# Optimization experiments

Measured on AMD Instinct MI355X. Metric: run time of the kernel, lower is better.

The kernel has to match this reference:

```python
import jax, jax.numpy as jnp
import numpy as np

B, S, D = 2, 2048, 1024
H, DK, DV = 16, 64, 64


def setup_inputs() -> dict:
    key = jax.random.key(0)
    ks = jax.random.split(key, 10)
    scale = 0.02
    return {
        "x": jax.random.normal(ks[0], (B, S, D), dtype=jnp.float32),
        "Wq": jax.random.normal(ks[1], (D, H * DK), dtype=jnp.float32) * scale,
        "bq": jax.random.normal(ks[2], (H * DK,), dtype=jnp.float32) * scale,
        "Wk": jax.random.normal(ks[3], (D, H * DK), dtype=jnp.float32) * scale,
        "bk": jax.random.normal(ks[4], (H * DK,), dtype=jnp.float32) * scale,
        "Wv": jax.random.normal(ks[5], (D, H * DV), dtype=jnp.float32) * scale,
        "bv": jax.random.normal(ks[6], (H * DV,), dtype=jnp.float32) * scale,
        "Wo": jax.random.normal(ks[7], (H * DV, D), dtype=jnp.float32) * scale,
        "bo": jax.random.normal(ks[8], (D,), dtype=jnp.float32) * scale,
    }


def reference(x, Wq, bq, Wk, bk, Wv, bv, Wo, bo):
    b, s, d = x.shape
    # projections -> (b, H, s, dk/dv)
    q = (x @ Wq + bq).reshape(b, s, H, DK).transpose(0, 2, 1, 3)
    k = (x @ Wk + bk).reshape(b, s, H, DK).transpose(0, 2, 1, 3)
    v = (x @ Wv + bv).reshape(b, s, H, DV).transpose(0, 2, 1, 3)
    # scaled QK^T: (b, H, s, s)
    scores = jnp.einsum("bhqd,bhkd->bhqk", q, k) / np.sqrt(DK).astype(np.float32)
    # sign-based reweighting: scores * sign(scores) (zeros -> sign 1) == |scores|
    reweighted = jnp.abs(scores)
    # causal mask: lower triangle keeps value, strict upper -> -inf (value * -inf)
    causal = jnp.tril(jnp.ones((s, s), dtype=bool))
    logits = jnp.where(causal, reweighted, -jnp.inf)
    w = jax.nn.softmax(logits, axis=-1)
    o = jnp.einsum("bhqk,bhkd->bhqd", w, v)  # (b, H, s, DV)
    o = o.transpose(0, 2, 1, 3).reshape(b, s, H * DV)
    return o @ Wo + bo
```

## Files before the change

kernel.cpp:

```cpp
#include <hip/hip_runtime.h>


#define DI __device__ __forceinline__

typedef __bf16 bf16x8 __attribute__((ext_vector_type(8)));
typedef float f32x4 __attribute__((ext_vector_type(4)));
typedef unsigned short u16x8 __attribute__((ext_vector_type(8)));
typedef unsigned short u16x4 __attribute__((ext_vector_type(4)));

union U8 { u16x8 u; bf16x8 b; };
union PB { unsigned int w[4]; u16x8 u; bf16x8 b; };

typedef const __attribute__((address_space(1))) unsigned int* gas_p;
typedef __attribute__((address_space(3))) unsigned int* las_p;

DI void gload16(const unsigned short* g, unsigned short* l) {
  __builtin_amdgcn_global_load_lds((gas_p)(const void*)g, (las_p)(void*)l, 16, 0, 0);
}

#define WAIT_VM4  asm volatile("s_waitcnt vmcnt(4)" ::: "memory")
#define WAIT_VM0  asm volatile("s_waitcnt vmcnt(0)" ::: "memory")
#define BARRIER   __builtin_amdgcn_s_barrier()

DI unsigned short f2bf(float f) {
  unsigned int u = __float_as_uint(f);
  u += 0x7FFFu + ((u >> 16) & 1u);
  return (unsigned short)(u >> 16);
}
DI float bf2f(unsigned short v) { return __uint_as_float((unsigned int)v << 16); }

__global__ __launch_bounds__(256) void k_conv_x(const float* __restrict__ x,
                                                unsigned short* __restrict__ xb) {
  size_t i = ((size_t)blockIdx.x * 256 + threadIdx.x) * 4;
  float4 v = *(const float4*)(x + i);
  u16x4 o;
  o[0] = f2bf(v.x); o[1] = f2bf(v.y); o[2] = f2bf(v.z); o[3] = f2bf(v.w);
  *(u16x4*)(xb + i) = o;
}

__global__ __launch_bounds__(256) void k_transpose(
    const float* __restrict__ W0, const float* __restrict__ W1,
    const float* __restrict__ W2, const float* __restrict__ W3,
    unsigned short* __restrict__ T0, unsigned short* __restrict__ T1,
    unsigned short* __restrict__ T2, unsigned short* __restrict__ T3) {
  const int z = blockIdx.z;
  const float* W = (z == 0) ? W0 : (z == 1) ? W1 : (z == 2) ? W2 : W3;
  unsigned short* T = (z == 0) ? T0 : (z == 1) ? T1 : (z == 2) ? T2 : T3;
  __shared__ unsigned short buf[32][33];
  const int k0 = blockIdx.x * 32, n0 = blockIdx.y * 32;
  const int tx = threadIdx.x, ty = threadIdx.y;
#pragma unroll
  for (int j = 0; j < 4; ++j) {
    int r = ty + j * 8;
    buf[r][tx] = f2bf(W[(size_t)(k0 + r) * 1024 + n0 + tx]);
  }
  __syncthreads();
#pragma unroll
  for (int j = 0; j < 4; ++j) {
    int c = ty + j * 8;
    T[(size_t)(n0 + c) * 1024 + k0 + tx] = buf[tx][c];
  }
}

DI void stage_gemm(const unsigned short* __restrict__ src, unsigned short* dst,
                   int row0, int k0, int tid, int wid) {
#pragma unroll
  for (int i = 0; i < 2; ++i) {
    int T = i * 256 + tid;
    int row = T >> 2, ch = T & 3;
    int sch = ch ^ (row & 3);
    gload16(&src[(size_t)(row0 + row) * 1024 + k0 + sch * 8],
            &dst[(i * 256 + wid * 64) * 8]);
  }
}

DI void gemm_main(const unsigned short* __restrict__ A,
                  const unsigned short* __restrict__ Bm,
                  unsigned short* As, unsigned short* Bs,
                  int m0, int n0, f32x4 acc[4][4]) {
  const int tid = threadIdx.x;
  const int lane = tid & 63, wid = tid >> 6;
  const int wr = wid >> 1, wc = wid & 1;
  const int g = lane >> 4, lq = lane & 15;

  stage_gemm(A, As, m0, 0, tid, wid);
  stage_gemm(Bm, Bs, n0, 0, tid, wid);
  __syncthreads();
  int buf = 0;
  for (int k0 = 0; k0 < 1024; k0 += 32) {
    if (k0 + 32 < 1024) {
      stage_gemm(A, As + (buf ^ 1) * 4096, m0, k0 + 32, tid, wid);
      stage_gemm(Bm, Bs + (buf ^ 1) * 4096, n0, k0 + 32, tid, wid);
    }
    const unsigned short* Ab = As + buf * 4096;
    const unsigned short* Bb = Bs + buf * 4096;
    U8 af[4], bfr[4];
#pragma unroll
    for (int f = 0; f < 4; ++f) {
      af[f].u  = *(const u16x8*)&Ab[(wr * 64 + f * 16 + lq) * 32 + ((g ^ (lq & 3)) * 8)];
      bfr[f].u = *(const u16x8*)&Bb[(wc * 64 + f * 16 + lq) * 32 + ((g ^ (lq & 3)) * 8)];
    }
#pragma unroll
    for (int i = 0; i < 4; ++i)
#pragma unroll
      for (int j = 0; j < 4; ++j)
        acc[i][j] = __builtin_amdgcn_mfma_f32_16x16x32_bf16(af[i].b, bfr[j].b,
                                                            acc[i][j], 0, 0, 0);
    __syncthreads();
    buf ^= 1;
  }
}

__global__ __launch_bounds__(256) void k_gemm_qkv(
    const unsigned short* __restrict__ xb,
    const unsigned short* __restrict__ Wqt, const unsigned short* __restrict__ Wkt,
    const unsigned short* __restrict__ Wvt,
    const float* __restrict__ bq, const float* __restrict__ bk,
    const float* __restrict__ bv,
    unsigned short* __restrict__ Qo, unsigned short* __restrict__ Ko,
    unsigned short* __restrict__ Vto) {
  __shared__ unsigned short Sh[128 * 136];
  unsigned short* As = Sh;
  unsigned short* Bs = Sh + 8192;
  const int z = blockIdx.z;
  const unsigned short* Bm = (z == 0) ? Wqt : (z == 1) ? Wkt : Wvt;
  const float* bias = (z == 0) ? bq : (z == 1) ? bk : bv;

  f32x4 acc[4][4];
#pragma unroll
  for (int i = 0; i < 4; ++i)
#pragma unroll
    for (int j = 0; j < 4; ++j) acc[i][j] = f32x4{0.f, 0.f, 0.f, 0.f};

  const int m0 = blockIdx.x * 128, n0 = blockIdx.y * 128;
  gemm_main(xb, Bm, As, Bs, m0, n0, acc);

  const int tid = threadIdx.x;
  const int lane = tid & 63, wid = tid >> 6;
  const int wr = wid >> 1, wc = wid & 1;
  const int g = lane >> 4, lq = lane & 15;
  const int bb = m0 >> 11;

#pragma unroll
  for (int j = 0; j < 4; ++j) {
    int col = wc * 64 + j * 16 + lq;
    float bv_ = bias[n0 + col];
#pragma unroll
    for (int i = 0; i < 4; ++i)
#pragma unroll
      for (int r = 0; r < 4; ++r) {
        int row = wr * 64 + i * 16 + g * 4 + r;
        Sh[row * 136 + col] = f2bf(acc[i][j][r] + bv_);
      }
  }
  __syncthreads();

  if (z < 2) {
    unsigned short* dstQK = (z == 0) ? Qo : Ko;
    const int ch = tid & 15, sb = tid >> 4;
#pragma unroll
    for (int it = 0; it < 8; ++it) {
      int s = sb + it * 16;
      u16x8 v = *(const u16x8*)&Sh[s * 136 + ch * 8];
      int gcol = n0 + ch * 8;
      int hh = gcol >> 6, dd = gcol & 63;
      int sr = (m0 + s) & 2047;
      *(u16x8*)&dstQK[(((size_t)(bb * 16 + hh)) * 2048 + sr) * 64 + dd] = v;
    }
  } else {
    const int d = tid & 127, hf = tid >> 7;
    int gcol = n0 + d;
    int hh = gcol >> 6, dd = gcol & 63;
    size_t vrow = ((size_t)(bb * 16 + hh)) * 64 + dd;
#pragma unroll
    for (int it = 0; it < 8; ++it) {
      int s0 = (hf + it * 2) * 8;
      u16x8 vv;
#pragma unroll
      for (int e = 0; e < 8; ++e) vv[e] = Sh[(s0 + e) * 136 + d];
      *(u16x8*)&Vto[vrow * 2048 + (m0 & 2047) + s0] = vv;
    }
  }
}

__global__ __launch_bounds__(256) void k_gemm_out(
    const unsigned short* __restrict__ Ob, const unsigned short* __restrict__ Wot,
    const float* __restrict__ bo, float* __restrict__ out) {
  __shared__ unsigned short As[2 * 4096];
  __shared__ unsigned short Bs[2 * 4096];
  f32x4 acc[4][4];
#pragma unroll
  for (int i = 0; i < 4; ++i)
#pragma unroll
    for (int j = 0; j < 4; ++j) acc[i][j] = f32x4{0.f, 0.f, 0.f, 0.f};

  const int m0 = blockIdx.x * 128, n0 = blockIdx.y * 128;
  gemm_main(Ob, Wot, As, Bs, m0, n0, acc);

  const int lane = threadIdx.x & 63, wid = threadIdx.x >> 6;
  const int wr = wid >> 1, wc = wid & 1;
  const int g = lane >> 4, lq = lane & 15;
#pragma unroll
  for (int j = 0; j < 4; ++j) {
    int col = n0 + wc * 64 + j * 16 + lq;
    float bv_ = bo[col];
#pragma unroll
    for (int i = 0; i < 4; ++i)
#pragma unroll
      for (int r = 0; r < 4; ++r) {
        int row = m0 + wr * 64 + i * 16 + g * 4 + r;
        out[(size_t)row * 1024 + col] = acc[i][j][r] + bv_;
      }
  }
}

template<bool MASKED>
DI void ptile(f32x4 sacc[4], f32x4& lacc, unsigned int pk[4][2],
              int qrow, int kk0, int g) {
  const float SC = 0.18033688011112042f;
#pragma unroll
  for (int c = 0; c < 4; ++c) {
#pragma unroll
    for (int r = 0; r < 4; ++r) {
      float sv = fabsf(sacc[c][r]) * SC;
      if (MASKED) {
        int k = kk0 + g * 8 + r + 4 * (c & 1) + 32 * (c >> 1);
        sv = (k <= qrow) ? sv : -1e30f;
      }
      float p = exp2f(sv);
      sacc[c][r] = p;
      lacc[r] += p;
    }
    asm("v_cvt_pk_bf16_f32 %0, %1, %2"
        : "=v"(pk[c][0]) : "v"(sacc[c][0]), "v"(sacc[c][1]));
    asm("v_cvt_pk_bf16_f32 %0, %1, %2"
        : "=v"(pk[c][1]) : "v"(sacc[c][2]), "v"(sacc[c][3]));
  }
}

DI void flash_dual(bool complete, int qblk, int t0, int t1, int slot,
                   const unsigned short* __restrict__ Q,
                   const unsigned short* __restrict__ Km,
                   const unsigned short* __restrict__ Vt,
                   unsigned short* __restrict__ O,
                   unsigned short* __restrict__ Pp, float* __restrict__ Lp,
                   unsigned short* Ks0, unsigned short* Vs0,
                   size_t qkbase, size_t vbase, int b, int h,
                   int tid, int wid, int g, int lq) {
  const int lrowA = wid * 32 + lq, lrowB = lrowA + 16;
  const int qrowA = qblk * 128 + lrowA, qrowB = qblk * 128 + lrowB;
  const int diag0 = 2 * qblk;

  auto stage = [&](int bf, int t) {
    const int kk0 = t * 64;
#pragma unroll
    for (int i = 0; i < 2; ++i) {
      int T = i * 256 + tid;
      int row = T >> 3, ch = T & 7;
      int sch = ch ^ (row & 7);
      gload16(&Km[qkbase + (size_t)(kk0 + row) * 64 + sch * 8],
              Ks0 + bf * 4096 + (i * 2048 + wid * 512));
      gload16(&Vt[vbase + (size_t)row * 2048 + kk0 + sch * 8],
              Vs0 + bf * 4096 + (i * 2048 + wid * 512));
    }
  };

  U8 aqA0, aqA1, aqB0, aqB1;
  {
    const unsigned short* qp = &Q[qkbase + (size_t)qrowA * 64 + g * 8];
    aqA0.u = *(const u16x8*)qp;
    aqA1.u = *(const u16x8*)(qp + 32);
    const unsigned short* qp2 = &Q[qkbase + (size_t)qrowB * 64 + g * 8];
    aqB0.u = *(const u16x8*)qp2;
    aqB1.u = *(const u16x8*)(qp2 + 32);
  }
  f32x4 laccA = f32x4{0.f, 0.f, 0.f, 0.f}, laccB = f32x4{0.f, 0.f, 0.f, 0.f};
  f32x4 oaccA[4], oaccB[4];
#pragma unroll
  for (int c = 0; c < 4; ++c) {
    oaccA[c] = f32x4{0.f, 0.f, 0.f, 0.f};
    oaccB[c] = f32x4{0.f, 0.f, 0.f, 0.f};
  }

  const int rbase = (lq >> 2) * 8 + (lq & 3);

  stage(0, t0);
  if (t0 + 1 < t1) stage(1, t0 + 1);
  int bi = 0;
  for (int t = t0; t < t1; ++t) {
    if (t + 1 < t1) WAIT_VM4; else WAIT_VM0;
    BARRIER;
    if (t + 2 < t1) {
      int nb = bi + 2; if (nb >= 3) nb -= 3;
      stage(nb, t + 2);
    }
    const unsigned short* Kb = Ks0 + bi * 4096;
    const unsigned short* Vb = Vs0 + bi * 4096;
    const int kk0 = t * 64;
    f32x4 saccA[4], saccB[4];
    __builtin_amdgcn_s_setprio(1);
#pragma unroll
    for (int c = 0; c < 4; ++c) {
      int row = rbase + 4 * (c & 1) + 32 * (c >> 1);
      int r7 = row & 7;
      U8 kf0, kf1;
      kf0.u = *(const u16x8*)&Kb[row * 64 + ((g ^ r7) * 8)];
      kf1.u = *(const u16x8*)&Kb[row * 64 + (((4 + g) ^ r7) * 8)];
      saccA[c] = __builtin_amdgcn_mfma_f32_16x16x32_bf16(kf0.b, aqA0.b,
                                                         f32x4{0.f, 0.f, 0.f, 0.f}, 0, 0, 0);
      saccA[c] = __builtin_amdgcn_mfma_f32_16x16x32_bf16(kf1.b, aqA1.b, saccA[c], 0, 0, 0);
      saccB[c] = __builtin_amdgcn_mfma_f32_16x16x32_bf16(kf0.b, aqB0.b,
                                                         f32x4{0.f, 0.f, 0.f, 0.f}, 0, 0, 0);
      saccB[c] = __builtin_amdgcn_mfma_f32_16x16x32_bf16(kf1.b, aqB1.b, saccB[c], 0, 0, 0);
    }
    __builtin_amdgcn_s_setprio(0);
    unsigned int pkA[4][2], pkB[4][2];
    if (t >= diag0) {
      ptile<true>(saccA, laccA, pkA, qrowA, kk0, g);
      ptile<true>(saccB, laccB, pkB, qrowB, kk0, g);
    } else {
      ptile<false>(saccA, laccA, pkA, qrowA, kk0, g);
      ptile<false>(saccB, laccB, pkB, qrowB, kk0, g);
    }
    __builtin_amdgcn_s_setprio(1);
#pragma unroll
    for (int hh = 0; hh < 2; ++hh) {
      PB pbA, pbB;
      pbA.w[0] = pkA[hh * 2 + 0][0]; pbA.w[1] = pkA[hh * 2 + 0][1];
      pbA.w[2] = pkA[hh * 2 + 1][0]; pbA.w[3] = pkA[hh * 2 + 1][1];
      pbB.w[0] = pkB[hh * 2 + 0][0]; pbB.w[1] = pkB[hh * 2 + 0][1];
      pbB.w[2] = pkB[hh * 2 + 1][0]; pbB.w[3] = pkB[hh * 2 + 1][1];
#pragma unroll
      for (int c = 0; c < 4; ++c) {
        U8 vf;
        vf.u = *(const u16x8*)&Vb[(c * 16 + lq) * 64 + (((hh * 4 + g) ^ (lq & 7)) * 8)];
        oaccA[c] = __builtin_amdgcn_mfma_f32_16x16x32_bf16(vf.b, pbA.b, oaccA[c], 0, 0, 0);
        oaccB[c] = __builtin_amdgcn_mfma_f32_16x16x32_bf16(vf.b, pbB.b, oaccB[c], 0, 0, 0);
      }
    }
    __builtin_amdgcn_s_setprio(0);
    ++bi; if (bi >= 3) bi = 0;
  }

  float lsA = (laccA[0] + laccA[1]) + (laccA[2] + laccA[3]);
  lsA += __shfl_xor(lsA, 16, 64);
  lsA += __shfl_xor(lsA, 32, 64);
  float lsB = (laccB[0] + laccB[1]) + (laccB[2] + laccB[3]);
  lsB += __shfl_xor(lsB, 16, 64);
  lsB += __shfl_xor(lsB, 32, 64);
  if (complete) {
    float invA = 1.0f / lsA, invB = 1.0f / lsB;
#pragma unroll
    for (int c = 0; c < 4; ++c) {
      u16x4 ovA, ovB;
#pragma unroll
      for (int r2 = 0; r2 < 4; ++r2) {
        ovA[r2] = f2bf(oaccA[c][r2] * invA);
        ovB[r2] = f2bf(oaccB[c][r2] * invB);
      }
      *(u16x4*)&O[((size_t)(b * 2048 + qrowA)) * 1024 + h * 64 + c * 16 + g * 4] = ovA;
      *(u16x4*)&O[((size_t)(b * 2048 + qrowB)) * 1024 + h * 64 + c * 16 + g * 4] = ovB;
    }
  } else {
    if (g == 0) {
      Lp[slot * 128 + lrowA] = lsA;
      Lp[slot * 128 + lrowB] = lsB;
    }
    size_t pbase = (size_t)slot * 8192;
#pragma unroll
    for (int c = 0; c < 4; ++c) {
      u16x4 ovA, ovB;
#pragma unroll
      for (int r2 = 0; r2 < 4; ++r2) {
        ovA[r2] = f2bf(oaccA[c][r2]);
        ovB[r2] = f2bf(oaccB[c][r2]);
      }
      *(u16x4*)&Pp[pbase + lrowA * 64 + c * 16 + g * 4] = ovA;
      *(u16x4*)&Pp[pbase + lrowB * 64 + c * 16 + g * 4] = ovB;
    }
  }
  WAIT_VM0;
  BARRIER;
}

__global__ __launch_bounds__(256) void k_flash(
    const unsigned short* __restrict__ Q, const unsigned short* __restrict__ Km,
    const unsigned short* __restrict__ Vt, unsigned short* __restrict__ O,
    unsigned short* __restrict__ Pp, float* __restrict__ Lp) {
  __shared__ unsigned short Ks[3 * 4096];
  __shared__ unsigned short Vs[3 * 4096];
  const int tid = threadIdx.x;
  const int lane = tid & 63, wid = tid >> 6;
  const int g = lane >> 4, lq = lane & 15;
  const int bid = blockIdx.x;
  const int xcd = bid & 7, idx = bid >> 3;
  const int bh = xcd * 4 + (idx >> 4);
  const int rr = idx & 15;
  const int p = rr >> 1, sp = rr & 1;
  const int mp = 15 - p;
  const int b = bh >> 4, h = bh & 15;
  const size_t qkbase = (size_t)bh * 2048 * 64;
  const size_t vbase = (size_t)bh * 64 * 2048;

  if (sp == 0) {
    flash_dual(true, p, 0, 2 * p + 2, 0, Q, Km, Vt, O, Pp, Lp,
               Ks, Vs, qkbase, vbase, b, h, tid, wid, g, lq);
    flash_dual(false, mp, 0, 15 - 2 * p, (bh * 8 + p) * 2 + 0, Q, Km, Vt, O, Pp, Lp,
               Ks, Vs, qkbase, vbase, b, h, tid, wid, g, lq);
  } else {
    flash_dual(false, mp, 15 - 2 * p, 32 - 2 * p, (bh * 8 + p) * 2 + 1, Q, Km, Vt, O, Pp, Lp,
               Ks, Vs, qkbase, vbase, b, h, tid, wid, g, lq);
  }
}

__global__ __launch_bounds__(256) void k_combine(
    const unsigned short* __restrict__ Pp, const float* __restrict__ Lp,
    unsigned short* __restrict__ O) {
  int gid = blockIdx.x * 256 + threadIdx.x;
  int dv4 = gid & 15;
  int q   = (gid >> 4) & 127;
  int pi  = (gid >> 11) & 7;
  int bh  = gid >> 14;
  int slot0 = (bh * 8 + pi) * 2;
  size_t base = (size_t)slot0 * 8192 + q * 64 + dv4 * 4;
  u16x4 a = *(const u16x4*)&Pp[base];
  u16x4 c = *(const u16x4*)&Pp[base + 8192];
  float l = Lp[slot0 * 128 + q] + Lp[(slot0 + 1) * 128 + q];
  float inv = 1.0f / l;
  u16x4 o;
#pragma unroll
  for (int r = 0; r < 4; ++r) o[r] = f2bf((bf2f(a[r]) + bf2f(c[r])) * inv);
  int b = bh >> 4, h = bh & 15;
  int srow = (15 - pi) * 128 + q;
  *(u16x4*)&O[((size_t)(b * 2048 + srow)) * 1024 + h * 64 + dv4 * 4] = o;
}

extern "C" void kernel_launch(void* const* d_in, const int* in_sizes, int n_in,
                              void* d_out, int out_size, void* d_ws, size_t ws_size,
                              hipStream_t stream) {
  const float* x  = (const float*)d_in[0];
  const float* Wq = (const float*)d_in[1];
  const float* bq = (const float*)d_in[2];
  const float* Wk = (const float*)d_in[3];
  const float* bk = (const float*)d_in[4];
  const float* Wv = (const float*)d_in[5];
  const float* bv = (const float*)d_in[6];
  const float* Wo = (const float*)d_in[7];
  const float* bo = (const float*)d_in[8];
  float* out = (float*)d_out;

  char* ws = (char*)d_ws;
  const size_t MB = 1024 * 1024;
  unsigned short* xb   = (unsigned short*)(ws + 0 * MB);
  unsigned short* Wqt  = (unsigned short*)(ws + 8 * MB);
  unsigned short* Wkt  = (unsigned short*)(ws + 10 * MB);
  unsigned short* Wvt  = (unsigned short*)(ws + 12 * MB);
  unsigned short* Wot  = (unsigned short*)(ws + 14 * MB);
  unsigned short* Qws  = (unsigned short*)(ws + 16 * MB);
  unsigned short* Kws  = (unsigned short*)(ws + 24 * MB);
  unsigned short* Vtws = (unsigned short*)(ws + 32 * MB);
  unsigned short* Ows  = (unsigned short*)(ws + 40 * MB);
  unsigned short* Pp   = (unsigned short*)(ws + 0 * MB);
  float*          Lp   = (float*)(ws + 8 * MB);

  k_conv_x<<<4096, 256, 0, stream>>>(x, xb);
  k_transpose<<<dim3(32, 32, 4), dim3(32, 8), 0, stream>>>(Wq, Wk, Wv, Wo,
                                                           Wqt, Wkt, Wvt, Wot);
  k_gemm_qkv<<<dim3(32, 8, 3), 256, 0, stream>>>(xb, Wqt, Wkt, Wvt, bq, bk, bv,
                                                 Qws, Kws, Vtws);
  k_flash<<<512, 256, 0, stream>>>(Qws, Kws, Vtws, Ows, Pp, Lp);
  k_combine<<<2048, 256, 0, stream>>>(Pp, Lp, Ows);
  k_gemm_out<<<dim3(32, 8), 256, 0, stream>>>(Ows, Wot, bo, out);
}
```

Measured before the change: 111.7 us.

## Fuse Q, K, V projections into one block sharing the staged x tile

The QKV GEMM kernel now computes all three projections in a single block, staging each x tile once and reusing it against the Wq, Wk and Wv tiles, which cuts x loads by a factor of three. The grid shrinks from 768 to 256 blocks and each thread holds 48 accumulator vectors, so register pressure rises and occupancy drops to one block per CU. On a GPU with 256 CUs this leaves a single wave of work, with less latency hiding. The epilogue stores the three outputs one after another through shared memory.

```diff
diff --git a/kernel.cpp b/kernel.cpp
--- a/kernel.cpp
+++ b/kernel.cpp
@@ -74,6 +74,115 @@
   }
 }
 
+__global__ __launch_bounds__(256, 1) void k_gemm_qkv(
+    const unsigned short* __restrict__ xb,
+    const unsigned short* __restrict__ Wqt, const unsigned short* __restrict__ Wkt,
+    const unsigned short* __restrict__ Wvt,
+    const float* __restrict__ bq, const float* __restrict__ bk,
+    const float* __restrict__ bv,
+    unsigned short* __restrict__ Qo, unsigned short* __restrict__ Ko,
+    unsigned short* __restrict__ Vto) {
+  __shared__ unsigned short Sh[4 * 8192];
+  unsigned short* As = Sh;
+  const unsigned short* Ws[3] = {Wqt, Wkt, Wvt};
+  const float* biases[3] = {bq, bk, bv};
+
+  f32x4 acc[3][4][4];
+#pragma unroll
+  for (int z = 0; z < 3; ++z)
+#pragma unroll
+    for (int i = 0; i < 4; ++i)
+#pragma unroll
+      for (int j = 0; j < 4; ++j) acc[z][i][j] = f32x4{0.f, 0.f, 0.f, 0.f};
+
+  const int m0 = blockIdx.x * 128, n0 = blockIdx.y * 128;
+  const int tid = threadIdx.x;
+  const int lane = tid & 63, wid = tid >> 6;
+  const int wr = wid >> 1, wc = wid & 1;
+  const int g = lane >> 4, lq = lane & 15;
+
+  stage_gemm(xb, As, m0, 0, tid, wid);
+#pragma unroll
+  for (int z = 0; z < 3; ++z)
+    stage_gemm(Ws[z], Sh + (1 + z) * 8192, n0, 0, tid, wid);
+  __syncthreads();
+  int buf = 0;
+  for (int k0 = 0; k0 < 1024; k0 += 32) {
+    if (k0 + 32 < 1024) {
+      stage_gemm(xb, As + (buf ^ 1) * 4096, m0, k0 + 32, tid, wid);
+#pragma unroll
+      for (int z = 0; z < 3; ++z)
+        stage_gemm(Ws[z], Sh + (1 + z) * 8192 + (buf ^ 1) * 4096, n0, k0 + 32, tid, wid);
+    }
+    const unsigned short* Ab = As + buf * 4096;
+    U8 af[4];
+#pragma unroll
+    for (int f = 0; f < 4; ++f)
+      af[f].u = *(const u16x8*)&Ab[(wr * 64 + f * 16 + lq) * 32 + ((g ^ (lq & 3)) * 8)];
+#pragma unroll
+    for (int z = 0; z < 3; ++z) {
+      const unsigned short* Bb = Sh + (1 + z) * 8192 + buf * 4096;
+      U8 bfr[4];
+#pragma unroll
+      for (int f = 0; f < 4; ++f)
+        bfr[f].u = *(const u16x8*)&Bb[(wc * 64 + f * 16 + lq) * 32 + ((g ^ (lq & 3)) * 8)];
+#pragma unroll
+      for (int i = 0; i < 4; ++i)
+#pragma unroll
+        for (int j = 0; j < 4; ++j)
+          acc[z][i][j] = __builtin_amdgcn_mfma_f32_16x16x32_bf16(af[i].b, bfr[j].b,
+                                                                 acc[z][i][j], 0, 0, 0);
+    }
+    __syncthreads();
+    buf ^= 1;
+  }
+
+  const int bb = m0 >> 11;
+#pragma unroll
+  for (int z = 0; z < 3; ++z) {
+#pragma unroll
+    for (int j = 0; j < 4; ++j) {
+      int col = wc * 64 + j * 16 + lq;
+      float bv_ = biases[z][n0 + col];
+#pragma unroll
+      for (int i = 0; i < 4; ++i)
+#pragma unroll
+        for (int r = 0; r < 4; ++r) {
+          int row = wr * 64 + i * 16 + g * 4 + r;
+          Sh[row * 136 + col] = f2bf(acc[z][i][j][r] + bv_);
+        }
+    }
+    __syncthreads();
+    if (z < 2) {
+      unsigned short* dstQK = (z == 0) ? Qo : Ko;
+      const int ch = tid & 15, sb = tid >> 4;
+#pragma unroll
+      for (int it = 0; it < 8; ++it) {
+        int s = sb + it * 16;
+        u16x8 v = *(const u16x8*)&Sh[s * 136 + ch * 8];
+        int gcol = n0 + ch * 8;
+        int hh = gcol >> 6, dd = gcol & 63;
+        int sr = (m0 + s) & 2047;
+        *(u16x8*)&dstQK[(((size_t)(bb * 16 + hh)) * 2048 + sr) * 64 + dd] = v;
+      }
+    } else {
+      const int d = tid & 127, hf = tid >> 7;
+      int gcol = n0 + d;
+      int hh = gcol >> 6, dd = gcol & 63;
+      size_t vrow = ((size_t)(bb * 16 + hh)) * 64 + dd;
+#pragma unroll
+      for (int it = 0; it < 8; ++it) {
+        int s0 = (hf + it * 2) * 8;
+        u16x8 vv;
+#pragma unroll
+        for (int e = 0; e < 8; ++e) vv[e] = Sh[(s0 + e) * 136 + d];
+        *(u16x8*)&Vto[vrow * 2048 + (m0 & 2047) + s0] = vv;
+      }
+    }
+    __syncthreads();
+  }
+}
+
 DI void gemm_main(const unsigned short* __restrict__ A,
                   const unsigned short* __restrict__ Bm,
                   unsigned short* As, unsigned short* Bs,
@@ -108,78 +217,6 @@
                                                             acc[i][j], 0, 0, 0);
     __syncthreads();
     buf ^= 1;
-  }
-}
-
-__global__ __launch_bounds__(256) void k_gemm_qkv(
-    const unsigned short* __restrict__ xb,
-    const unsigned short* __restrict__ Wqt, const unsigned short* __restrict__ Wkt,
-    const unsigned short* __restrict__ Wvt,
-    const float* __restrict__ bq, const float* __restrict__ bk,
-    const float* __restrict__ bv,
-    unsigned short* __restrict__ Qo, unsigned short* __restrict__ Ko,
-    unsigned short* __restrict__ Vto) {
-  __shared__ unsigned short Sh[128 * 136];
-  unsigned short* As = Sh;
-  unsigned short* Bs = Sh + 8192;
-  const int z = blockIdx.z;
-  const unsigned short* Bm = (z == 0) ? Wqt : (z == 1) ? Wkt : Wvt;
-  const float* bias = (z == 0) ? bq : (z == 1) ? bk : bv;
-
-  f32x4 acc[4][4];
-#pragma unroll
-  for (int i = 0; i < 4; ++i)
-#pragma unroll
-    for (int j = 0; j < 4; ++j) acc[i][j] = f32x4{0.f, 0.f, 0.f, 0.f};
-
-  const int m0 = blockIdx.x * 128, n0 = blockIdx.y * 128;
-  gemm_main(xb, Bm, As, Bs, m0, n0, acc);
-
-  const int tid = threadIdx.x;
-  const int lane = tid & 63, wid = tid >> 6;
-  const int wr = wid >> 1, wc = wid & 1;
-  const int g = lane >> 4, lq = lane & 15;
-  const int bb = m0 >> 11;
-
-#pragma unroll
-  for (int j = 0; j < 4; ++j) {
-    int col = wc * 64 + j * 16 + lq;
-    float bv_ = bias[n0 + col];
-#pragma unroll
-    for (int i = 0; i < 4; ++i)
-#pragma unroll
-      for (int r = 0; r < 4; ++r) {
-        int row = wr * 64 + i * 16 + g * 4 + r;
-        Sh[row * 136 + col] = f2bf(acc[i][j][r] + bv_);
-      }
-  }
-  __syncthreads();
-
-  if (z < 2) {
-    unsigned short* dstQK = (z == 0) ? Qo : Ko;
-    const int ch = tid & 15, sb = tid >> 4;
-#pragma unroll
-    for (int it = 0; it < 8; ++it) {
-      int s = sb + it * 16;
-      u16x8 v = *(const u16x8*)&Sh[s * 136 + ch * 8];
-      int gcol = n0 + ch * 8;
-      int hh = gcol >> 6, dd = gcol & 63;
-      int sr = (m0 + s) & 2047;
-      *(u16x8*)&dstQK[(((size_t)(bb * 16 + hh)) * 2048 + sr) * 64 + dd] = v;
-    }
-  } else {
-    const int d = tid & 127, hf = tid >> 7;
-    int gcol = n0 + d;
-    int hh = gcol >> 6, dd = gcol & 63;
-    size_t vrow = ((size_t)(bb * 16 + hh)) * 64 + dd;
-#pragma unroll
-    for (int it = 0; it < 8; ++it) {
-      int s0 = (hf + it * 2) * 8;
-      u16x8 vv;
-#pragma unroll
-      for (int e = 0; e < 8; ++e) vv[e] = Sh[(s0 + e) * 136 + d];
-      *(u16x8*)&Vto[vrow * 2048 + (m0 & 2047) + s0] = vv;
-    }
   }
 }
 
@@ -466,8 +503,8 @@
   k_conv_x<<<4096, 256, 0, stream>>>(x, xb);
   k_transpose<<<dim3(32, 32, 4), dim3(32, 8), 0, stream>>>(Wq, Wk, Wv, Wo,
                                                            Wqt, Wkt, Wvt, Wot);
-  k_gemm_qkv<<<dim3(32, 8, 3), 256, 0, stream>>>(xb, Wqt, Wkt, Wvt, bq, bk, bv,
-                                                 Qws, Kws, Vtws);
+  k_gemm_qkv<<<dim3(32, 8), 256, 0, stream>>>(xb, Wqt, Wkt, Wvt, bq, bk, bv,
+                                              Qws, Kws, Vtws);
   k_flash<<<512, 256, 0, stream>>>(Qws, Kws, Vtws, Ows, Pp, Lp);
   k_combine<<<2048, 256, 0, stream>>>(Pp, Lp, Ows);
   k_gemm_out<<<dim3(32, 8), 256, 0, stream>>>(Ows, Wot, bo, out);
```

Result: slower. 117.6 us (+5.3%).
